# Kernel tuning notes

Measured on AMD Instinct MI355X. Metric: run time of the kernel, lower is better.

## Reference

```python
import jax, jax.numpy as jnp
import numpy as np

T = 512           # num_timestamps
D = 512           # video_embed_dim
V = 2048          # fmri_dim (voxels)
H = 128           # hidden_dim


def setup_inputs() -> dict:
    key = jax.random.key(0)
    k = jax.random.split(key, 8)
    s1 = 1.0 / np.sqrt(D)
    s2 = 1.0 / np.sqrt(H)
    return {
        "video_embeddings": jax.random.normal(k[0], (T, D), dtype=jnp.float32),
        # stacked per-voxel weights (torch Linear: y = x @ W.T + b; we store W already transposed as [in, out])
        "W1": jax.random.uniform(k[1], (V, D, H), jnp.float32, -s1, s1),
        "b1": jax.random.uniform(k[2], (V, H), jnp.float32, -s1, s1),
        "W2": jax.random.uniform(k[3], (V, H, H), jnp.float32, -s2, s2),
        "b2": jax.random.uniform(k[4], (V, H), jnp.float32, -s2, s2),
        "W3": jax.random.uniform(k[5], (V, H), jnp.float32, -s2, s2),
        "b3": jax.random.uniform(k[6], (V,), jnp.float32, -s2, s2),
    }


def reference(video_embeddings, W1, b1, W2, b2, W3, b3):
    # Per-voxel MLP expressed as batched GEMMs over the voxel axis.
    # Dropout is identity in eval mode.
    h = jax.nn.relu(jnp.einsum("td,vdh->tvh", video_embeddings, W1) + b1)  # [T,V,H]
    h = jax.nn.relu(jnp.einsum("tvh,vhg->tvg", h, W2) + b2)                 # [T,V,H]
    out = jnp.einsum("tvh,vh->tv", h, W3) + b3                               # [T,V]
    return out
```

## Files before the change

### kernel.cpp

```cpp
#include <hip/hip_runtime.h>
#include <hip/hip_bf16.h>

#define TT 512
#define DD 512
#define VV 2048
#define HH 128

typedef __attribute__((ext_vector_type(8))) short bf16x8;
typedef __attribute__((ext_vector_type(8))) unsigned short ushort8;
typedef __attribute__((ext_vector_type(4))) unsigned short ushort4v;
typedef __attribute__((ext_vector_type(4))) float f32x4;

__device__ __forceinline__ unsigned short f2bf(float f) {
  union { __hip_bfloat16 b; unsigned short u; } cv;
  cv.b = __float2bfloat16(f);
  return cv.u;
}

__device__ __forceinline__ void lds_barrier() {
  asm volatile("s_waitcnt lgkmcnt(0)\n\ts_barrier" ::: "memory");
}

#define VM_GATE(N)                                                   \
  do {                                                               \
    asm volatile("s_waitcnt vmcnt(" #N ")" ::: "memory");            \
    __builtin_amdgcn_sched_barrier(0);                               \
  } while (0)

__global__ void cvt_x_kernel(const float* __restrict__ x, unsigned short* __restrict__ xb) {
  const int i = blockIdx.x * blockDim.x + threadIdx.x;
  const float4 f = ((const float4*)x)[i];
  ushort4v u;
  u[0] = f2bf(f.x); u[1] = f2bf(f.y); u[2] = f2bf(f.z); u[3] = f2bf(f.w);
  ((ushort4v*)xb)[i] = u;
}

__global__ __launch_bounds__(512, 4)
void voxel_mlp_kernel(const unsigned short* __restrict__ Xb,
                      const float* __restrict__ W1,
                      const float* __restrict__ b1,
                      const float* __restrict__ W2,
                      const float* __restrict__ b2,
                      const float* __restrict__ W3,
                      const float* __restrict__ b3,
                      float* __restrict__ out) {
  __shared__ __align__(16) char LDS[65536];
  constexpr unsigned GBASE  = 0;
  constexpr unsigned FBASE  = 49152;
  constexpr unsigned W2BASE = 0;
  constexpr unsigned H1BASE = 32768;

  const int bid  = blockIdx.x;
  const int xcd  = bid & 7;
  const int gg   = bid >> 3;
  const int half = gg & 1;
  const int v    = (gg >> 1) * 8 + xcd;

  const int tid = threadIdx.x;
  const int w   = tid >> 6;
  const int l   = tid & 63;
  const int lg  = l >> 4;
  const int ll  = l & 15;

  const float* W1v = W1 + (size_t)v * DD * HH;
  const float* W2v = W2 + (size_t)v * HH * HH;

  const size_t gsrc = (size_t)((w * 4 + (l >> 5)) * HH + (l & 31) * 4);
  const int n_c = l >> 3;
  const int ll0 = (l & 7) * 2;

#define G_ISSUE(t)                                                          \
  { const float* gp = W1v + (size_t)(t) * 32 * HH + gsrc;                   \
    const unsigned ldst = GBASE + (unsigned)((t) % 3) * 16384u +            \
                          (unsigned)w * 2048u;                              \
    _Pragma("unroll") for (int p = 0; p < 2; ++p)                           \
      __builtin_amdgcn_global_load_lds(                                     \
        (const __attribute__((address_space(1))) void*)(gp + p * 2 * HH),   \
        (__attribute__((address_space(3))) void*)(&LDS[ldst + p * 1024u]),  \
        16, 0, 0); }

#define CVT(tau)                                                            \
  { const unsigned gs = GBASE + (unsigned)((tau) % 3) * 16384u;             \
    ushort4v ev, ov;                                                        \
    _Pragma("unroll") for (int r = 0; r < 4; ++r) {                         \
      const float2 g2 = *(const float2*)(&LDS[gs +                          \
          (unsigned)((w * 4 + r) * 512 + (n_c * 16 + ll0) * 4)]);           \
      ev[r] = f2bf(g2.x); ov[r] = f2bf(g2.y); }                             \
    const unsigned fb = FBASE + (unsigned)((tau) & 1) * 8192u +             \
                        (unsigned)n_c * 1024u;                              \
    const unsigned ca = (unsigned)((((w >> 1) * 16 + ll0) * 16) ^ (n_c << 4)); \
    const unsigned cb = (unsigned)((((w >> 1) * 16 + ll0 + 1) * 16) ^ (n_c << 4)); \
    *(ushort4v*)(&LDS[fb + ca + (unsigned)(w & 1) * 8u]) = ev;              \
    *(ushort4v*)(&LDS[fb + cb + (unsigned)(w & 1) * 8u]) = ov; }

  G_ISSUE(0);
  G_ISSUE(1);
  VM_GATE(2);
  CVT(0);
  lds_barrier();

  f32x4 acc1[2][8];
#pragma unroll
  for (int mi = 0; mi < 2; ++mi)
#pragma unroll
    for (int n = 0; n < 8; ++n) acc1[mi][n] = f32x4{0.f, 0.f, 0.f, 0.f};

#pragma unroll
  for (int s = 0; s < 16; ++s) {
    bf16x8 aF[2];
#pragma unroll
    for (int mi = 0; mi < 2; ++mi)
      aF[mi] = *(const bf16x8*)(Xb + (size_t)(half * 256 + w * 32 + mi * 16 + ll) * DD +
                                s * 32 + lg * 8);
    __builtin_amdgcn_sched_barrier(0);

    if (s < 14) {
      G_ISSUE(s + 2);
      VM_GATE(2);
    } else if (s == 14) {
      VM_GATE(0);
    }

    if (s < 15) CVT(s + 1);

#pragma unroll
    for (int n = 0; n < 8; ++n) {
      const bf16x8 b = *(const bf16x8*)(&LDS[FBASE + (unsigned)(s & 1) * 8192u +
                                             (unsigned)n * 1024u +
                                             (unsigned)(((lg * 16 + ll) * 16) ^ (n << 4))]);
#pragma unroll
      for (int mi = 0; mi < 2; ++mi)
        acc1[mi][n] = __builtin_amdgcn_mfma_f32_16x16x32_bf16(aF[mi], b, acc1[mi][n], 0, 0, 0);
    }
    lds_barrier();
  }
#undef G_ISSUE
#undef CVT

  float b1v[8], b2v[8], w3v[8];
#pragma unroll
  for (int n = 0; n < 8; ++n) {
    b1v[n] = b1[v * HH + n * 16 + ll];
    b2v[n] = b2[v * HH + n * 16 + ll];
    w3v[n] = W3[v * HH + n * 16 + ll];
  }
  const float b3v = b3[v];

  {
    const int ki = w & 3, mb = (w >> 2) * 4;
    float w2t[4][8];
#pragma unroll
    for (int q = 0; q < 4; ++q)
#pragma unroll
      for (int j = 0; j < 8; ++j)
        w2t[q][j] = W2v[(ki * 32 + lg * 8 + j) * HH + (mb + q) * 16 + ll];
#pragma unroll
    for (int q = 0; q < 4; ++q) {
      ushort8 e;
#pragma unroll
      for (int j = 0; j < 8; ++j) e[j] = f2bf(w2t[q][j]);
      *(ushort8*)(&LDS[W2BASE + (unsigned)ki * 8192u + (unsigned)(mb + q) * 1024u +
                       (unsigned)l * 16u]) = e;
    }
  }
  lds_barrier();

  const unsigned slot = H1BASE + (unsigned)w * 4096u;

#pragma unroll
  for (int mi = 0; mi < 2; ++mi) {
#pragma unroll
    for (int n = 0; n < 8; ++n) {
#pragma unroll
      for (int r = 0; r < 4; ++r) {
        const int tl = lg * 4 + r;
        float hv = acc1[mi][n][r] + b1v[n];
        hv = fmaxf(hv, 0.f);
        const int h = n * 16 + ll;
        const unsigned byte = slot + (unsigned)tl * 256u +
                              (unsigned)((h * 2) ^ ((tl & 7) << 4));
        *(unsigned short*)(&LDS[byte]) = f2bf(hv);
      }
    }
    f32x4 acc2[8];
#pragma unroll
    for (int m = 0; m < 8; ++m) acc2[m] = f32x4{0.f, 0.f, 0.f, 0.f};
#pragma unroll
    for (int ki = 0; ki < 4; ++ki) {
      const int k0 = ki * 32 + lg * 8;
      const unsigned abyte = slot + (unsigned)ll * 256u +
                             (unsigned)((k0 * 2) ^ ((ll & 7) << 4));
      const bf16x8 a2 = *(const bf16x8*)(&LDS[abyte]);
#pragma unroll
      for (int m = 0; m < 8; ++m) {
        const bf16x8 bw = *(const bf16x8*)(&LDS[W2BASE + (unsigned)ki * 8192u +
                                                (unsigned)m * 1024u + (unsigned)l * 16u]);
        acc2[m] = __builtin_amdgcn_mfma_f32_16x16x32_bf16(a2, bw, acc2[m], 0, 0, 0);
      }
    }
#pragma unroll
    for (int r = 0; r < 4; ++r) {
      float p = 0.f;
#pragma unroll
      for (int m = 0; m < 8; ++m)
        p += fmaxf(acc2[m][r] + b2v[m], 0.f) * w3v[m];
      p += __shfl_xor(p, 1);
      p += __shfl_xor(p, 2);
      p += __shfl_xor(p, 4);
      p += __shfl_xor(p, 8);
      if (ll == 0) {
        const int t = half * 256 + w * 32 + mi * 16 + lg * 4 + r;
        out[t * VV + v] = p + b3v;
      }
    }
  }
}

extern "C" void kernel_launch(void* const* d_in, const int* in_sizes, int n_in,
                              void* d_out, int out_size, void* d_ws, size_t ws_size,
                              hipStream_t stream) {
  const float* X  = (const float*)d_in[0];
  const float* W1 = (const float*)d_in[1];
  const float* b1 = (const float*)d_in[2];
  const float* W2 = (const float*)d_in[3];
  const float* b2 = (const float*)d_in[4];
  const float* W3 = (const float*)d_in[5];
  const float* b3 = (const float*)d_in[6];
  float* out = (float*)d_out;

  unsigned short* Xb = (unsigned short*)d_ws;

  cvt_x_kernel<<<256, 256, 0, stream>>>(X, Xb);
  voxel_mlp_kernel<<<VV * 2, 512, 0, stream>>>(Xb, W1, b1, W2, b2, W3, b3, out);
}
```

Baseline: 343.5 us.

## Halve block to 256 threads with 64 rows per wave and double-buffered padded W1 staging

Shrinks each block from 8 to 4 waves. Each wave now covers 64 timestep rows (4 M-tiles), so every B fragment loaded from LDS feeds more MFMAs. W1 staging changes from a triple buffer to a double buffer with a 1040-byte padded row stride, and the fp32-to-bf16 conversion now uses plain round-to-nearest bit arithmetic into an unswizzled fragment layout. An extra barrier is added per step, and the larger accumulator array raises register pressure, which limits occupancy.

```diff
diff --git a/kernel.cpp b/kernel.cpp
--- a/kernel.cpp
+++ b/kernel.cpp
@@ -35,7 +35,7 @@
   ((ushort4v*)xb)[i] = u;
 }
 
-__global__ __launch_bounds__(512, 4)
+__global__ __launch_bounds__(256, 2)
 void voxel_mlp_kernel(const unsigned short* __restrict__ Xb,
                       const float* __restrict__ W1,
                       const float* __restrict__ b1,
@@ -44,9 +44,10 @@
                       const float* __restrict__ W3,
                       const float* __restrict__ b3,
                       float* __restrict__ out) {
-  __shared__ __align__(16) char LDS[65536];
+  __shared__ __align__(16) char LDS[49664];
   constexpr unsigned GBASE  = 0;
-  constexpr unsigned FBASE  = 49152;
+  constexpr unsigned GSLOT  = 16640;
+  constexpr unsigned FBASE  = 33280;
   constexpr unsigned W2BASE = 0;
   constexpr unsigned H1BASE = 32768;
 
@@ -65,71 +66,67 @@
   const float* W1v = W1 + (size_t)v * DD * HH;
   const float* W2v = W2 + (size_t)v * HH * HH;
 
-  const size_t gsrc = (size_t)((w * 4 + (l >> 5)) * HH + (l & 31) * 4);
-  const int n_c = l >> 3;
-  const int ll0 = (l & 7) * 2;
+  const size_t gsrc = (size_t)(w * 8) * HH + (size_t)l * 4;
 
 #define G_ISSUE(t)                                                          \
   { const float* gp = W1v + (size_t)(t) * 32 * HH + gsrc;                   \
-    const unsigned ldst = GBASE + (unsigned)((t) % 3) * 16384u +            \
-                          (unsigned)w * 2048u;                              \
-    _Pragma("unroll") for (int p = 0; p < 2; ++p)                           \
+    const unsigned ld0 = GBASE + (unsigned)((t) & 1) * GSLOT +              \
+                         (unsigned)(w * 4) * 1040u;                         \
+    _Pragma("unroll") for (int p = 0; p < 4; ++p)                           \
       __builtin_amdgcn_global_load_lds(                                     \
         (const __attribute__((address_space(1))) void*)(gp + p * 2 * HH),   \
-        (__attribute__((address_space(3))) void*)(&LDS[ldst + p * 1024u]),  \
+        (__attribute__((address_space(3))) void*)(&LDS[ld0 + (unsigned)p * 1040u]), \
         16, 0, 0); }
 
 #define CVT(tau)                                                            \
-  { const unsigned gs = GBASE + (unsigned)((tau) % 3) * 16384u;             \
-    ushort4v ev, ov;                                                        \
-    _Pragma("unroll") for (int r = 0; r < 4; ++r) {                         \
-      const float2 g2 = *(const float2*)(&LDS[gs +                          \
-          (unsigned)((w * 4 + r) * 512 + (n_c * 16 + ll0) * 4)]);           \
-      ev[r] = f2bf(g2.x); ov[r] = f2bf(g2.y); }                             \
-    const unsigned fb = FBASE + (unsigned)((tau) & 1) * 8192u +             \
-                        (unsigned)n_c * 1024u;                              \
-    const unsigned ca = (unsigned)((((w >> 1) * 16 + ll0) * 16) ^ (n_c << 4)); \
-    const unsigned cb = (unsigned)((((w >> 1) * 16 + ll0 + 1) * 16) ^ (n_c << 4)); \
-    *(ushort4v*)(&LDS[fb + ca + (unsigned)(w & 1) * 8u]) = ev;              \
-    *(ushort4v*)(&LDS[fb + cb + (unsigned)(w & 1) * 8u]) = ov; }
+  { const unsigned gs = GBASE + (unsigned)((tau) & 1) * GSLOT;              \
+    _Pragma("unroll") for (int p = 0; p < 2; ++p) {                         \
+      const int n = w + p * 4;                                              \
+      ushort8 e;                                                            \
+      _Pragma("unroll") for (int j = 0; j < 8; ++j) {                       \
+        const int k = lg * 8 + j;                                           \
+        const unsigned u = *(const unsigned*)(&LDS[gs +                     \
+            (unsigned)((k >> 1) * 1040 + (k & 1) * 512 + (n * 16 + ll) * 4)]); \
+        e[j] = (unsigned short)((u + 0x8000u) >> 16);                       \
+      }                                                                     \
+      *(ushort8*)(&LDS[FBASE + (unsigned)((tau) & 1) * 8192u +              \
+                       (unsigned)n * 1024u + (unsigned)l * 16u]) = e;       \
+    } }
 
   G_ISSUE(0);
   G_ISSUE(1);
-  VM_GATE(2);
+  VM_GATE(4);
+  lds_barrier();
   CVT(0);
   lds_barrier();
 
-  f32x4 acc1[2][8];
-#pragma unroll
-  for (int mi = 0; mi < 2; ++mi)
+  f32x4 acc1[4][8];
+#pragma unroll
+  for (int mi = 0; mi < 4; ++mi)
 #pragma unroll
     for (int n = 0; n < 8; ++n) acc1[mi][n] = f32x4{0.f, 0.f, 0.f, 0.f};
 
 #pragma unroll
   for (int s = 0; s < 16; ++s) {
-    bf16x8 aF[2];
-#pragma unroll
-    for (int mi = 0; mi < 2; ++mi)
-      aF[mi] = *(const bf16x8*)(Xb + (size_t)(half * 256 + w * 32 + mi * 16 + ll) * DD +
+    bf16x8 aF[4];
+#pragma unroll
+    for (int mi = 0; mi < 4; ++mi)
+      aF[mi] = *(const bf16x8*)(Xb + (size_t)(half * 256 + w * 64 + mi * 16 + ll) * DD +
                                 s * 32 + lg * 8);
     __builtin_amdgcn_sched_barrier(0);
 
-    if (s < 14) {
-      G_ISSUE(s + 2);
-      VM_GATE(2);
-    } else if (s == 14) {
-      VM_GATE(0);
-    }
+    if (s < 14) G_ISSUE(s + 2);
+    VM_GATE(4);
+    lds_barrier();
 
     if (s < 15) CVT(s + 1);
 
 #pragma unroll
     for (int n = 0; n < 8; ++n) {
       const bf16x8 b = *(const bf16x8*)(&LDS[FBASE + (unsigned)(s & 1) * 8192u +
-                                             (unsigned)n * 1024u +
-                                             (unsigned)(((lg * 16 + ll) * 16) ^ (n << 4))]);
-#pragma unroll
-      for (int mi = 0; mi < 2; ++mi)
+                                             (unsigned)n * 1024u + (unsigned)l * 16u]);
+#pragma unroll
+      for (int mi = 0; mi < 4; ++mi)
         acc1[mi][n] = __builtin_amdgcn_mfma_f32_16x16x32_bf16(aF[mi], b, acc1[mi][n], 0, 0, 0);
     }
     lds_barrier();
@@ -146,20 +143,20 @@
   }
   const float b3v = b3[v];
 
-  {
-    const int ki = w & 3, mb = (w >> 2) * 4;
+#pragma unroll
+  for (int pass = 0; pass < 2; ++pass) {
     float w2t[4][8];
 #pragma unroll
     for (int q = 0; q < 4; ++q)
 #pragma unroll
       for (int j = 0; j < 8; ++j)
-        w2t[q][j] = W2v[(ki * 32 + lg * 8 + j) * HH + (mb + q) * 16 + ll];
+        w2t[q][j] = W2v[(w * 32 + lg * 8 + j) * HH + (pass * 4 + q) * 16 + ll];
 #pragma unroll
     for (int q = 0; q < 4; ++q) {
       ushort8 e;
 #pragma unroll
       for (int j = 0; j < 8; ++j) e[j] = f2bf(w2t[q][j]);
-      *(ushort8*)(&LDS[W2BASE + (unsigned)ki * 8192u + (unsigned)(mb + q) * 1024u +
+      *(ushort8*)(&LDS[W2BASE + (unsigned)w * 8192u + (unsigned)(pass * 4 + q) * 1024u +
                        (unsigned)l * 16u]) = e;
     }
   }
@@ -168,7 +165,7 @@
   const unsigned slot = H1BASE + (unsigned)w * 4096u;
 
 #pragma unroll
-  for (int mi = 0; mi < 2; ++mi) {
+  for (int mi = 0; mi < 4; ++mi) {
 #pragma unroll
     for (int n = 0; n < 8; ++n) {
 #pragma unroll
@@ -209,7 +206,7 @@
       p += __shfl_xor(p, 4);
       p += __shfl_xor(p, 8);
       if (ll == 0) {
-        const int t = half * 256 + w * 32 + mi * 16 + lg * 4 + r;
+        const int t = half * 256 + w * 64 + mi * 16 + lg * 4 + r;
         out[t * VV + v] = p + b3v;
       }
     }
@@ -231,5 +228,5 @@
   unsigned short* Xb = (unsigned short*)d_ws;
 
   cvt_x_kernel<<<256, 256, 0, stream>>>(X, Xb);
-  voxel_mlp_kernel<<<VV * 2, 512, 0, stream>>>(Xb, W1, b1, W2, b2, W3, b3, out);
-}
+  voxel_mlp_kernel<<<VV * 2, 256, 0, stream>>>(Xb, W1, b1, W2, b2, W3, b3, out);
+}
```

Result: faster. 293.1 us (-14.7%).
